# Performance work log

Measured on AMD Instinct MI355X. Metric: run time of the kernel, lower is better.

## Reference

```python
import jax, jax.numpy as jnp
import numpy as np


def _rbf_forward(batches, centers, beta, W, b):
    # Pairwise Euclidean distances via GEMM expansion instead of materializing
    # the O(n*K*dim) difference tensor the torch code builds.
    x2 = jnp.sum(batches * batches, axis=1, keepdims=True)          # [n, 1]
    c2 = jnp.sum(centers * centers, axis=1)                          # [K]
    xc = jnp.einsum('nd,kd->nk', batches, centers)                   # [n, K]
    d2 = jnp.maximum(x2 + c2[None, :] - 2.0 * xc, 0.0)               # [n, K]
    dist = jnp.sqrt(d2)
    radial = jnp.exp(-beta * dist)                                   # beta: [1, K]
    return radial @ W.T + b                                          # [n, num_class]


def setup_inputs() -> dict:
    key = jax.random.key(0)
    k1, k2, k3, k4, k5 = jax.random.split(key, 5)
    n, K, dim, num_class = 16384, 2048, 512, 10
    batches = jax.random.normal(k1, (n, dim), dtype=jnp.float32)
    centers = jax.random.normal(k2, (K, dim), dtype=jnp.float32)
    beta = jnp.full((1, K), 0.1, dtype=jnp.float32)  # torch init: ones/10
    W = jax.random.normal(k4, (num_class, K), dtype=jnp.float32) / np.sqrt(K)
    b = jax.random.normal(k5, (num_class,), dtype=jnp.float32) * 0.01
    return {"batches": batches, "centers": centers, "beta": beta, "W": W, "b": b}


def reference(batches, centers, beta, W, b):
    return _rbf_forward(batches, centers, beta, W, b)
```

## Files before the change

kernel.cpp:

```cpp
#include <hip/hip_runtime.h>
#include <hip/hip_bf16.h>
#include <stdint.h>

#define M_N  16384
#define K_C  2048
#define DIM  512
#define NCLS 10
#define NBN  (K_C / 128)

typedef unsigned short u16;
typedef float  f32x4  __attribute__((ext_vector_type(4)));
typedef __bf16 bf16x8 __attribute__((ext_vector_type(8)));


__device__ __forceinline__ void async_ld16(const void* g, void* l) {
  __builtin_amdgcn_global_load_lds(
      (const __attribute__((address_space(1))) void*)g,
      (__attribute__((address_space(3))) void*)l,
      16, 0, 0);
}

__device__ __forceinline__ u16 f2bf_rne(float f) {
  uint32_t u = __float_as_uint(f);
  u += 0x7FFFu + ((u >> 16) & 1u);
  return (u16)(u >> 16);
}


__global__ void convert_rows(const float4* __restrict__ src,
                             ushort4* __restrict__ dst,
                             float* __restrict__ sq) {
  int row = blockIdx.x;
  int t = threadIdx.x;
  float4 v = src[(size_t)row * 128 + t];
  float ss = v.x * v.x + v.y * v.y + v.z * v.z + v.w * v.w;
  ushort4 o;
  o.x = f2bf_rne(v.x); o.y = f2bf_rne(v.y);
  o.z = f2bf_rne(v.z); o.w = f2bf_rne(v.w);
  dst[(size_t)row * 128 + t] = o;
  ss += __shfl_down(ss, 32);
  ss += __shfl_down(ss, 16);
  ss += __shfl_down(ss, 8);
  ss += __shfl_down(ss, 4);
  ss += __shfl_down(ss, 2);
  ss += __shfl_down(ss, 1);
  __shared__ float part[2];
  if ((t & 63) == 0) part[t >> 6] = ss;
  __syncthreads();
  if (t == 0) sq[row] = part[0] + part[1];
}


__global__ __launch_bounds__(256, 2) void rbf_main(
    const u16* __restrict__ A,
    const u16* __restrict__ B,
    const float* __restrict__ x2,
    const float* __restrict__ c2,
    const float* __restrict__ beta,
    const float* __restrict__ W,
    float* __restrict__ partial) {
  constexpr int BM = 128, BK = 64;
  constexpr int RLD = BM + 4;
  __shared__ alignas(16) unsigned char smem[128 * RLD * 2];
  u16* As = (u16*)smem;
  u16* Bs = (u16*)(smem + 16384);
  u16* Rt = (u16*)smem;

  const int tid  = threadIdx.x;
  const int lane = tid & 63;
  const int wid  = tid >> 6;
  const int bn = blockIdx.x, bm = blockIdx.y;
  const int row0 = bm * BM, col0 = bn * 128;
  const int wr = (wid >> 1) * 64;
  const int wc = (wid & 1) * 64;

  f32x4 acc[4][4] = {};

  const int srow = tid >> 3;
  const int scol = (tid & 7) * 8;
  const u16* aG = A + (size_t)(row0 + srow) * DIM + scol;
  const u16* bG = B + (size_t)(col0 + srow) * DIM + scol;
  u16* aL = As + tid * 8;
  u16* bL = Bs + tid * 8;

  const int frow = lane & 15;
  const int fko  = (lane >> 4) * 8;

  for (int k0 = 0; k0 < DIM; k0 += BK) {
    __syncthreads();
#pragma unroll
    for (int i = 0; i < 4; ++i) {
      async_ld16(aG + k0 + i * 32 * DIM, aL + i * 2048);
      async_ld16(bG + k0 + i * 32 * DIM, bL + i * 2048);
    }
    __syncthreads();

#pragma unroll
    for (int kh = 0; kh < 2; ++kh) {
      bf16x8 af[4], bfr[4];
#pragma unroll
      for (int mi = 0; mi < 4; ++mi)
        af[mi] = *(const bf16x8*)(As + (wr + mi * 16 + frow) * BK + kh * 32 + fko);
#pragma unroll
      for (int ni = 0; ni < 4; ++ni)
        bfr[ni] = *(const bf16x8*)(Bs + (wc + ni * 16 + frow) * BK + kh * 32 + fko);
#pragma unroll
      for (int mi = 0; mi < 4; ++mi)
#pragma unroll
        for (int ni = 0; ni < 4; ++ni)
          acc[mi][ni] = __builtin_amdgcn_mfma_f32_16x16x32_bf16(
              af[mi], bfr[ni], acc[mi][ni], 0, 0, 0);
    }
  }

  float c2v[4], btv[4];
#pragma unroll
  for (int ni = 0; ni < 4; ++ni) {
    int gc = col0 + wc + ni * 16 + (lane & 15);
    c2v[ni] = c2[gc];
    btv[ni] = beta[gc];
  }
  float x2v[4][4];
#pragma unroll
  for (int mi = 0; mi < 4; ++mi)
#pragma unroll
    for (int r = 0; r < 4; ++r)
      x2v[mi][r] = x2[row0 + wr + mi * 16 + (lane >> 4) * 4 + r];

  __syncthreads();

  union Pack { u16 h[4]; uint2 v; };
#pragma unroll
  for (int mi = 0; mi < 4; ++mi) {
#pragma unroll
    for (int ni = 0; ni < 4; ++ni) {
      Pack pk;
#pragma unroll
      for (int r = 0; r < 4; ++r) {
        float xc = acc[mi][ni][r];
        float d2 = fmaxf(x2v[mi][r] + c2v[ni] - 2.0f * xc, 0.0f);
        float radial = __expf(-btv[ni] * sqrtf(d2));
        pk.h[r] = f2bf_rne(radial);
      }
      int ccol = wc + ni * 16 + (lane & 15);
      int rrow = wr + mi * 16 + (lane >> 4) * 4;
      *(uint2*)(Rt + ccol * RLD + rrow) = pk.v;
    }
  }
  __syncthreads();

  const int r  = tid & 127;
  const int jh = tid >> 7;
  float accj[5] = {};
  for (int c = 0; c < 128; ++c) {
    uint32_t bits = (uint32_t)Rt[c * RLD + r];
    float v = __uint_as_float(bits << 16);
    int gc = col0 + c;
#pragma unroll
    for (int jj = 0; jj < 5; ++jj)
      accj[jj] += v * W[(jh * 5 + jj) * K_C + gc];
  }
  float* dst = partial + (size_t)bn * (M_N * NCLS)
             + (size_t)(row0 + r) * NCLS + jh * 5;
#pragma unroll
  for (int jj = 0; jj < 5; ++jj) dst[jj] = accj[jj];
}


__global__ void reduce_out(const float* __restrict__ partial,
                           const float* __restrict__ b,
                           float* __restrict__ out) {
  int idx = blockIdx.x * 256 + threadIdx.x;
  if (idx >= M_N * NCLS) return;
  float s = b[idx % NCLS];
#pragma unroll
  for (int bn = 0; bn < NBN; ++bn)
    s += partial[(size_t)bn * (M_N * NCLS) + idx];
  out[idx] = s;
}


extern "C" void kernel_launch(void* const* d_in, const int* in_sizes, int n_in,
                              void* d_out, int out_size, void* d_ws, size_t ws_size,
                              hipStream_t stream) {
  const float* batches = (const float*)d_in[0];
  const float* centers = (const float*)d_in[1];
  const float* beta    = (const float*)d_in[2];
  const float* W       = (const float*)d_in[3];
  const float* bias    = (const float*)d_in[4];
  float* out = (float*)d_out;

  char* ws = (char*)d_ws;
  u16*  Abf = (u16*)ws;
  u16*  Bbf = (u16*)(ws + (size_t)M_N * DIM * 2);
  float* x2 = (float*)(ws + (size_t)M_N * DIM * 2 + (size_t)K_C * DIM * 2);
  float* c2 = x2 + M_N;
  float* partial = c2 + K_C;

  convert_rows<<<dim3(M_N), dim3(128), 0, stream>>>(
      (const float4*)batches, (ushort4*)Abf, x2);
  convert_rows<<<dim3(K_C), dim3(128), 0, stream>>>(
      (const float4*)centers, (ushort4*)Bbf, c2);
  rbf_main<<<dim3(NBN, M_N / 128), dim3(256), 0, stream>>>(
      Abf, Bbf, x2, c2, beta, W, partial);
  reduce_out<<<dim3((M_N * NCLS + 255) / 256), dim3(256), 0, stream>>>(
      partial, bias, out);
}
```

Baseline: 163.2 us.

## Swizzle LDS tiles, raise occupancy, and use one wave per row in convert

The main GEMM kernel now XOR-swizzles the 16-byte column slots of the A/B LDS tiles on both the async-load and fragment-read sides, to cut LDS bank conflicts on the MFMA operand loads. Launch bounds go from 2 to 4 blocks per SM to raise occupancy, which tightens the register budget and risks spills with the 4x4 accumulator tile. The convert kernel now uses one wavefront per row with two float4 per lane, which removes the shared-memory reduction and the block barrier. The W projection loop is rewritten with explicit scalar loads.

```diff
diff --git a/kernel.cpp b/kernel.cpp
--- a/kernel.cpp
+++ b/kernel.cpp
@@ -27,31 +27,33 @@
 }
 
 
-__global__ void convert_rows(const float4* __restrict__ src,
-                             ushort4* __restrict__ dst,
-                             float* __restrict__ sq) {
-  int row = blockIdx.x;
-  int t = threadIdx.x;
-  float4 v = src[(size_t)row * 128 + t];
-  float ss = v.x * v.x + v.y * v.y + v.z * v.z + v.w * v.w;
-  ushort4 o;
-  o.x = f2bf_rne(v.x); o.y = f2bf_rne(v.y);
-  o.z = f2bf_rne(v.z); o.w = f2bf_rne(v.w);
-  dst[(size_t)row * 128 + t] = o;
+__global__ __launch_bounds__(256) void convert_rows(
+    const float4* __restrict__ src, ushort4* __restrict__ dst,
+    float* __restrict__ sq, int nrows) {
+  int lane = threadIdx.x & 63;
+  int row = blockIdx.x * 4 + (threadIdx.x >> 6);
+  if (row >= nrows) return;
+  float ss = 0.f;
+#pragma unroll
+  for (int i = 0; i < 2; ++i) {
+    float4 v = src[(size_t)row * 128 + lane * 2 + i];
+    ss += v.x * v.x + v.y * v.y + v.z * v.z + v.w * v.w;
+    ushort4 o;
+    o.x = f2bf_rne(v.x); o.y = f2bf_rne(v.y);
+    o.z = f2bf_rne(v.z); o.w = f2bf_rne(v.w);
+    dst[(size_t)row * 128 + lane * 2 + i] = o;
+  }
   ss += __shfl_down(ss, 32);
   ss += __shfl_down(ss, 16);
   ss += __shfl_down(ss, 8);
   ss += __shfl_down(ss, 4);
   ss += __shfl_down(ss, 2);
   ss += __shfl_down(ss, 1);
-  __shared__ float part[2];
-  if ((t & 63) == 0) part[t >> 6] = ss;
-  __syncthreads();
-  if (t == 0) sq[row] = part[0] + part[1];
-}
-
-
-__global__ __launch_bounds__(256, 2) void rbf_main(
+  if (lane == 0) sq[row] = ss;
+}
+
+
+__global__ __launch_bounds__(256, 4) void rbf_main(
     const u16* __restrict__ A,
     const u16* __restrict__ B,
     const float* __restrict__ x2,
@@ -59,8 +61,8 @@
     const float* __restrict__ beta,
     const float* __restrict__ W,
     float* __restrict__ partial) {
-  constexpr int BM = 128, BK = 64;
-  constexpr int RLD = BM + 4;
+  constexpr int BK = 64;
+  constexpr int RLD = 128 + 4;
   __shared__ alignas(16) unsigned char smem[128 * RLD * 2];
   u16* As = (u16*)smem;
   u16* Bs = (u16*)(smem + 16384);
@@ -70,21 +72,22 @@
   const int lane = tid & 63;
   const int wid  = tid >> 6;
   const int bn = blockIdx.x, bm = blockIdx.y;
-  const int row0 = bm * BM, col0 = bn * 128;
+  const int row0 = bm * 128, col0 = bn * 128;
   const int wr = (wid >> 1) * 64;
   const int wc = (wid & 1) * 64;
 
   f32x4 acc[4][4] = {};
 
   const int srow = tid >> 3;
-  const int scol = (tid & 7) * 8;
+  const int scol = ((tid & 7) ^ (srow & 7)) * 8;
   const u16* aG = A + (size_t)(row0 + srow) * DIM + scol;
   const u16* bG = B + (size_t)(col0 + srow) * DIM + scol;
   u16* aL = As + tid * 8;
   u16* bL = Bs + tid * 8;
 
   const int frow = lane & 15;
-  const int fko  = (lane >> 4) * 8;
+  const int fq   = lane >> 4;
+  const int fsw  = frow & 7;
 
   for (int k0 = 0; k0 < DIM; k0 += BK) {
     __syncthreads();
@@ -97,13 +100,14 @@
 
 #pragma unroll
     for (int kh = 0; kh < 2; ++kh) {
+      const int slot = ((kh << 2) | fq) ^ fsw;
       bf16x8 af[4], bfr[4];
 #pragma unroll
       for (int mi = 0; mi < 4; ++mi)
-        af[mi] = *(const bf16x8*)(As + (wr + mi * 16 + frow) * BK + kh * 32 + fko);
+        af[mi] = *(const bf16x8*)(As + (wr + mi * 16 + frow) * BK + slot * 8);
 #pragma unroll
       for (int ni = 0; ni < 4; ++ni)
-        bfr[ni] = *(const bf16x8*)(Bs + (wc + ni * 16 + frow) * BK + kh * 32 + fko);
+        bfr[ni] = *(const bf16x8*)(Bs + (wc + ni * 16 + frow) * BK + slot * 8);
 #pragma unroll
       for (int mi = 0; mi < 4; ++mi)
 #pragma unroll
@@ -151,19 +155,21 @@
 
   const int r  = tid & 127;
   const int jh = tid >> 7;
-  float accj[5] = {};
+  float2 a01 = {0.f, 0.f}, a23 = {0.f, 0.f};
+  float a4 = 0.f;
   for (int c = 0; c < 128; ++c) {
     uint32_t bits = (uint32_t)Rt[c * RLD + r];
     float v = __uint_as_float(bits << 16);
-    int gc = col0 + c;
-#pragma unroll
-    for (int jj = 0; jj < 5; ++jj)
-      accj[jj] += v * W[(jh * 5 + jj) * K_C + gc];
+    int gw = jh * 5 * K_C + col0 + c;
+    float w0 = W[gw], w1 = W[gw + K_C], w2 = W[gw + 2 * K_C],
+          w3 = W[gw + 3 * K_C], w4 = W[gw + 4 * K_C];
+    a01.x += v * w0; a01.y += v * w1;
+    a23.x += v * w2; a23.y += v * w3;
+    a4 += v * w4;
   }
   float* dst = partial + (size_t)bn * (M_N * NCLS)
              + (size_t)(row0 + r) * NCLS + jh * 5;
-#pragma unroll
-  for (int jj = 0; jj < 5; ++jj) dst[jj] = accj[jj];
+  dst[0] = a01.x; dst[1] = a01.y; dst[2] = a23.x; dst[3] = a23.y; dst[4] = a4;
 }
 
 
@@ -197,10 +203,10 @@
   float* c2 = x2 + M_N;
   float* partial = c2 + K_C;
 
-  convert_rows<<<dim3(M_N), dim3(128), 0, stream>>>(
-      (const float4*)batches, (ushort4*)Abf, x2);
-  convert_rows<<<dim3(K_C), dim3(128), 0, stream>>>(
-      (const float4*)centers, (ushort4*)Bbf, c2);
+  convert_rows<<<dim3(M_N / 4), dim3(256), 0, stream>>>(
+      (const float4*)batches, (ushort4*)Abf, x2, M_N);
+  convert_rows<<<dim3(K_C / 4), dim3(256), 0, stream>>>(
+      (const float4*)centers, (ushort4*)Bbf, c2, K_C);
   rbf_main<<<dim3(NBN, M_N / 128), dim3(256), 0, stream>>>(
       Abf, Bbf, x2, c2, beta, W, partial);
   reduce_out<<<dim3((M_N * NCLS + 255) / 256), dim3(256), 0, stream>>>(
```

New measurement: 164.2 us. Within noise of the previous version (+0.6%).

## Use MFMA for radial-by-W projection, swizzle LDS, transpose GEMM tile roles

Applied to the files above, without the earlier changes.

The radial @ W^T step moves from a scalar per-thread loop over 128 columns to bf16 MFMA instructions, using a bf16 copy of W padded to 16 classes and produced by a new conversion kernel. The main GEMM swaps the A/B operand roles so each accumulator holds centers along rows, and applies XOR swizzling to the LDS layouts of both the operand tiles and the radial tile to avoid bank conflicts. Launch bounds are raised to 4 blocks per CU and the partial-sum layout becomes row-major with 16 classes per tile, which also changes the reduce kernel. W is now rounded to bf16, which adds rounding error to the final projection.

```diff
diff --git a/kernel.cpp b/kernel.cpp
--- a/kernel.cpp
+++ b/kernel.cpp
@@ -51,17 +51,24 @@
 }
 
 
-__global__ __launch_bounds__(256, 2) void rbf_main(
+__global__ void convert_w(const float* __restrict__ W, u16* __restrict__ Wbf) {
+  int idx = blockIdx.x * 256 + threadIdx.x;
+  int n = idx >> 11, k = idx & 2047;
+  float v = (n < NCLS) ? W[n * K_C + k] : 0.0f;
+  Wbf[idx] = f2bf_rne(v);
+}
+
+
+__global__ __launch_bounds__(256, 4) void rbf_main(
     const u16* __restrict__ A,
     const u16* __restrict__ B,
     const float* __restrict__ x2,
     const float* __restrict__ c2,
     const float* __restrict__ beta,
-    const float* __restrict__ W,
+    const u16* __restrict__ Wbf,
     float* __restrict__ partial) {
-  constexpr int BM = 128, BK = 64;
-  constexpr int RLD = BM + 4;
-  __shared__ alignas(16) unsigned char smem[128 * RLD * 2];
+  constexpr int BK = 64;
+  __shared__ alignas(16) unsigned char smem[32768];
   u16* As = (u16*)smem;
   u16* Bs = (u16*)(smem + 16384);
   u16* Rt = (u16*)smem;
@@ -70,21 +77,22 @@
   const int lane = tid & 63;
   const int wid  = tid >> 6;
   const int bn = blockIdx.x, bm = blockIdx.y;
-  const int row0 = bm * BM, col0 = bn * 128;
-  const int wr = (wid >> 1) * 64;
-  const int wc = (wid & 1) * 64;
+  const int row0 = bm * 128, col0 = bn * 128;
+  const int wrC = (wid >> 1) * 64;
+  const int wcB = (wid & 1) * 64;
 
   f32x4 acc[4][4] = {};
 
   const int srow = tid >> 3;
-  const int scol = (tid & 7) * 8;
+  const int scol = ((tid & 7) ^ (srow & 7)) * 8;
   const u16* aG = A + (size_t)(row0 + srow) * DIM + scol;
   const u16* bG = B + (size_t)(col0 + srow) * DIM + scol;
   u16* aL = As + tid * 8;
   u16* bL = Bs + tid * 8;
 
   const int frow = lane & 15;
-  const int fko  = (lane >> 4) * 8;
+  const int fq   = lane >> 4;
+  const int fsw  = frow & 7;
 
   for (int k0 = 0; k0 < DIM; k0 += BK) {
     __syncthreads();
@@ -97,35 +105,40 @@
 
 #pragma unroll
     for (int kh = 0; kh < 2; ++kh) {
-      bf16x8 af[4], bfr[4];
+      const int slot = ((kh << 2) | fq) ^ fsw;
+      bf16x8 cf[4], bfr[4];
 #pragma unroll
       for (int mi = 0; mi < 4; ++mi)
-        af[mi] = *(const bf16x8*)(As + (wr + mi * 16 + frow) * BK + kh * 32 + fko);
+        cf[mi] = *(const bf16x8*)(Bs + (wrC + mi * 16 + frow) * BK + slot * 8);
 #pragma unroll
       for (int ni = 0; ni < 4; ++ni)
-        bfr[ni] = *(const bf16x8*)(Bs + (wc + ni * 16 + frow) * BK + kh * 32 + fko);
+        bfr[ni] = *(const bf16x8*)(As + (wcB + ni * 16 + frow) * BK + slot * 8);
 #pragma unroll
       for (int mi = 0; mi < 4; ++mi)
 #pragma unroll
         for (int ni = 0; ni < 4; ++ni)
           acc[mi][ni] = __builtin_amdgcn_mfma_f32_16x16x32_bf16(
-              af[mi], bfr[ni], acc[mi][ni], 0, 0, 0);
-    }
-  }
-
-  float c2v[4], btv[4];
-#pragma unroll
-  for (int ni = 0; ni < 4; ++ni) {
-    int gc = col0 + wc + ni * 16 + (lane & 15);
-    c2v[ni] = c2[gc];
-    btv[ni] = beta[gc];
-  }
-  float x2v[4][4];
-#pragma unroll
-  for (int mi = 0; mi < 4; ++mi)
-#pragma unroll
-    for (int r = 0; r < 4; ++r)
-      x2v[mi][r] = x2[row0 + wr + mi * 16 + (lane >> 4) * 4 + r];
+              cf[mi], bfr[ni], acc[mi][ni], 0, 0, 0);
+    }
+  }
+
+  const int cls = lane & 15, q = lane >> 4;
+  bf16x8 wfr[4];
+#pragma unroll
+  for (int t = 0; t < 4; ++t)
+    wfr[t] = *(const bf16x8*)(Wbf + (size_t)cls * K_C + col0 + t * 32 + q * 8);
+
+  float4 c2q[4], btq[4];
+#pragma unroll
+  for (int mi = 0; mi < 4; ++mi) {
+    int base = col0 + wrC + mi * 16 + q * 4;
+    c2q[mi] = *(const float4*)(c2 + base);
+    btq[mi] = *(const float4*)(beta + base);
+  }
+  float x2v[4];
+#pragma unroll
+  for (int ni = 0; ni < 4; ++ni)
+    x2v[ni] = x2[row0 + wcB + ni * 16 + cls];
 
   __syncthreads();
 
@@ -138,32 +151,38 @@
 #pragma unroll
       for (int r = 0; r < 4; ++r) {
         float xc = acc[mi][ni][r];
-        float d2 = fmaxf(x2v[mi][r] + c2v[ni] - 2.0f * xc, 0.0f);
-        float radial = __expf(-btv[ni] * sqrtf(d2));
+        float d2 = fmaxf(x2v[ni] + c2q[mi][r] - 2.0f * xc, 0.0f);
+        float radial = __expf(-btq[mi][r] * sqrtf(d2));
         pk.h[r] = f2bf_rne(radial);
       }
-      int ccol = wc + ni * 16 + (lane & 15);
-      int rrow = wr + mi * 16 + (lane >> 4) * 4;
-      *(uint2*)(Rt + ccol * RLD + rrow) = pk.v;
+      int br  = wcB + ni * 16 + cls;
+      int cc0 = wrC + mi * 16 + q * 4;
+      *(uint2*)(Rt + br * 128 + (cc0 ^ ((br & 15) << 3))) = pk.v;
     }
   }
   __syncthreads();
 
-  const int r  = tid & 127;
-  const int jh = tid >> 7;
-  float accj[5] = {};
-  for (int c = 0; c < 128; ++c) {
-    uint32_t bits = (uint32_t)Rt[c * RLD + r];
-    float v = __uint_as_float(bits << 16);
-    int gc = col0 + c;
-#pragma unroll
-    for (int jj = 0; jj < 5; ++jj)
-      accj[jj] += v * W[(jh * 5 + jj) * K_C + gc];
-  }
-  float* dst = partial + (size_t)bn * (M_N * NCLS)
-             + (size_t)(row0 + r) * NCLS + jh * 5;
-#pragma unroll
-  for (int jj = 0; jj < 5; ++jj) dst[jj] = accj[jj];
+  f32x4 acc2[2] = {};
+#pragma unroll
+  for (int s2 = 0; s2 < 2; ++s2) {
+    const int br = (wid * 2 + s2) * 16 + cls;
+    const u16* rrow = Rt + br * 128;
+    const int sw = cls << 3;
+#pragma unroll
+    for (int t = 0; t < 4; ++t) {
+      bf16x8 ra = *(const bf16x8*)(rrow + ((t * 32 + q * 8) ^ sw));
+      acc2[s2] = __builtin_amdgcn_mfma_f32_16x16x32_bf16(
+          ra, wfr[t], acc2[s2], 0, 0, 0);
+    }
+  }
+
+#pragma unroll
+  for (int s2 = 0; s2 < 2; ++s2)
+#pragma unroll
+    for (int r = 0; r < 4; ++r) {
+      int gr = row0 + (wid * 2 + s2) * 16 + q * 4 + r;
+      partial[(size_t)gr * (NBN * 16) + bn * 16 + cls] = acc2[s2][r];
+    }
 }
 
 
@@ -172,10 +191,11 @@
                            float* __restrict__ out) {
   int idx = blockIdx.x * 256 + threadIdx.x;
   if (idx >= M_N * NCLS) return;
-  float s = b[idx % NCLS];
-#pragma unroll
-  for (int bn = 0; bn < NBN; ++bn)
-    s += partial[(size_t)bn * (M_N * NCLS) + idx];
+  int i = idx / NCLS, j = idx - i * NCLS;
+  float s = b[j];
+  const float* p = partial + (size_t)i * (NBN * 16) + j;
+#pragma unroll
+  for (int bn = 0; bn < NBN; ++bn) s += p[bn * 16];
   out[idx] = s;
 }
 
@@ -193,16 +213,18 @@
   char* ws = (char*)d_ws;
   u16*  Abf = (u16*)ws;
   u16*  Bbf = (u16*)(ws + (size_t)M_N * DIM * 2);
-  float* x2 = (float*)(ws + (size_t)M_N * DIM * 2 + (size_t)K_C * DIM * 2);
+  float* x2 = (float*)(ws + (size_t)(M_N + K_C) * DIM * 2);
   float* c2 = x2 + M_N;
-  float* partial = c2 + K_C;
+  u16*  Wbf = (u16*)(c2 + K_C);
+  float* partial = (float*)((char*)Wbf + 16 * K_C * 2);
 
   convert_rows<<<dim3(M_N), dim3(128), 0, stream>>>(
       (const float4*)batches, (ushort4*)Abf, x2);
   convert_rows<<<dim3(K_C), dim3(128), 0, stream>>>(
       (const float4*)centers, (ushort4*)Bbf, c2);
+  convert_w<<<dim3(16 * K_C / 256), dim3(256), 0, stream>>>(W, Wbf);
   rbf_main<<<dim3(NBN, M_N / 128), dim3(256), 0, stream>>>(
-      Abf, Bbf, x2, c2, beta, W, partial);
+      Abf, Bbf, x2, c2, beta, Wbf, partial);
   reduce_out<<<dim3((M_N * NCLS + 255) / 256), dim3(256), 0, stream>>>(
       partial, bias, out);
 }
```

Result: faster. 147.8 us (-9.5%).
